# Kernel tuning notes

Hardware: AMD Instinct MI355X
Metric: run time of the kernel (lower is better)

Reference implementation:

```python
import jax, jax.numpy as jnp
import numpy as np

N = 50000      # nodes
E = 800000     # edges (before self-loops)
F_IN = 256     # num_features
H = 8          # heads (conv1)
C = 32         # hidden_size per head (conv1)
OUT = 2        # conv2 out channels (1 head)
NEG_SLOPE = 0.2


def setup_inputs() -> dict:
    key = jax.random.key(0)
    ks = jax.random.split(key, 12)
    x = jax.random.normal(ks[0], (N, F_IN), jnp.float32)
    edge_index = jax.random.randint(ks[1], (2, E), 0, N, dtype=jnp.int64)

    def glorot(k, shape):
        fan = shape[0] if len(shape) == 2 else int(np.prod(shape))
        s = float(np.sqrt(6.0 / (fan + shape[-1])))
        return jax.random.uniform(k, shape, jnp.float32, -s, s)

    W1 = glorot(ks[2], (F_IN, H * C))
    att_src1 = glorot(ks[3], (H, C))
    att_dst1 = glorot(ks[4], (H, C))
    b1 = jnp.zeros((H * C,), jnp.float32)
    W2 = glorot(ks[5], (H * C, 1 * OUT))
    att_src2 = glorot(ks[6], (1, OUT))
    att_dst2 = glorot(ks[7], (1, OUT))
    b2 = jnp.zeros((OUT,), jnp.float32)
    return {"x": x, "edge_index": edge_index, "W1": W1, "att_src1": att_src1,
            "att_dst1": att_dst1, "b1": b1, "W2": W2, "att_src2": att_src2,
            "att_dst2": att_dst2, "b2": b2}


def gat_conv(x, src, dst, W, a_src, a_dst, b, heads, ch, n):
    # x: [n, f] -> projected [n, heads, ch]
    xp = (x @ W).reshape(n, heads, ch)
    alpha_src = jnp.einsum('nhc,hc->nh', xp, a_src)   # [n, H]
    alpha_dst = jnp.einsum('nhc,hc->nh', xp, a_dst)   # [n, H]
    e = jax.nn.leaky_relu(alpha_src[src] + alpha_dst[dst], NEG_SLOPE)  # [E', H]
    # segment softmax over edges grouped by destination node
    m = jax.ops.segment_max(e, dst, num_segments=n)                    # [n, H]
    p = jnp.exp(e - m[dst])
    denom = jax.ops.segment_sum(p, dst, num_segments=n)                # [n, H]
    alpha = p / denom[dst]                                             # [E', H]
    # weighted scatter-aggregate of source messages
    out = jax.ops.segment_sum(xp[src] * alpha[:, :, None], dst, num_segments=n)
    return out.reshape(n, heads * ch) + b


def reference(x, edge_index, W1, att_src1, att_dst1, b1, W2, att_src2, att_dst2, b2):
    n = x.shape[0]
    loops = jnp.arange(n, dtype=edge_index.dtype)  # GATConv add_self_loops=True
    src = jnp.concatenate([edge_index[0], loops])
    dst = jnp.concatenate([edge_index[1], loops])
    h = jax.nn.relu(gat_conv(x, src, dst, W1, att_src1, att_dst1, b1, H, C, n))
    # eval mode: F.dropout and attention dropout are identity
    return gat_conv(h, src, dst, W2, att_src2, att_dst2, b2, 1, OUT, n)
```

## Files before the change

kernel.cpp:

```cpp
#include <hip/hip_runtime.h>
#include <math.h>

#define N_NODES 50000
#define N_EDGES 800000
#define EP (N_EDGES + N_NODES)
#define NEG 0.2f
#define SCAN_BLOCKS 49

typedef __attribute__((ext_vector_type(8))) short bf16x8;
typedef __attribute__((ext_vector_type(4))) float f32x4;

static __device__ __forceinline__ unsigned short bf16_rn(float f) {
    union { float f; unsigned int u; } v; v.f = f;
    unsigned int u = v.u;
    unsigned int r = (u + 0x7FFFu + ((u >> 16) & 1u)) >> 16;
    return (unsigned short)r;
}
static __device__ __forceinline__ float bf16_tof(unsigned short u) {
    union { unsigned int u; float f; } v; v.u = ((unsigned int)u) << 16;
    return v.f;
}


__global__ void k_hist(const int* __restrict__ ei, int* __restrict__ counts) {
    int e = blockIdx.x * 256 + threadIdx.x;
    if (e >= EP) return;
    int d = (e < N_EDGES) ? ei[N_EDGES + e] : (e - N_EDGES);
    atomicAdd(&counts[d], 1);
}

__global__ void k_scan_block(const int* __restrict__ counts, int* __restrict__ excl,
                             int* __restrict__ bsums) {
    __shared__ int wsum[4];
    int b = blockIdx.x, t = threadIdx.x;
    int lane = t & 63, w = t >> 6;
    int i0 = b * 1024 + t * 4;
    int v0 = (i0 + 0 < N_NODES) ? counts[i0 + 0] : 0;
    int v1 = (i0 + 1 < N_NODES) ? counts[i0 + 1] : 0;
    int v2 = (i0 + 2 < N_NODES) ? counts[i0 + 2] : 0;
    int v3 = (i0 + 3 < N_NODES) ? counts[i0 + 3] : 0;
    int s = v0 + v1 + v2 + v3;
    int incl = s;
    #pragma unroll
    for (int d = 1; d < 64; d <<= 1) {
        int u = __shfl_up(incl, d);
        if (lane >= d) incl += u;
    }
    if (lane == 63) wsum[w] = incl;
    __syncthreads();
    if (t == 0) {
        int run = 0;
        #pragma unroll
        for (int i = 0; i < 4; ++i) { int x = wsum[i]; wsum[i] = run; run += x; }
        bsums[b] = run;
    }
    __syncthreads();
    int base = wsum[w] + incl - s;
    if (i0 + 0 < N_NODES) excl[i0 + 0] = base;
    if (i0 + 1 < N_NODES) excl[i0 + 1] = base + v0;
    if (i0 + 2 < N_NODES) excl[i0 + 2] = base + v0 + v1;
    if (i0 + 3 < N_NODES) excl[i0 + 3] = base + v0 + v1 + v2;
}

__global__ void k_scan_mid(int* __restrict__ bsums) {
    int t = threadIdx.x;
    int v = (t < SCAN_BLOCKS) ? bsums[t] : 0;
    int incl = v;
    #pragma unroll
    for (int d = 1; d < 64; d <<= 1) {
        int u = __shfl_up(incl, d);
        if (t >= d) incl += u;
    }
    if (t < SCAN_BLOCKS) bsums[t] = incl - v;
}

__global__ void k_scan_add(int* __restrict__ row_ptr, const int* __restrict__ bsums) {
    int b = blockIdx.x, t = threadIdx.x;
    int off = bsums[b];
    int i0 = b * 1024 + t * 4;
    #pragma unroll
    for (int j = 0; j < 4; ++j)
        if (i0 + j < N_NODES) row_ptr[i0 + j] += off;
    if (b == 0 && t == 0) row_ptr[N_NODES] = EP;
}

__global__ void k_scatter(const int* __restrict__ ei, const int* __restrict__ row_ptr,
                          int* __restrict__ fill, int* __restrict__ colb) {
    int e = blockIdx.x * 256 + threadIdx.x;
    if (e >= EP) return;
    int s, d;
    if (e < N_EDGES) { s = ei[e]; d = ei[N_EDGES + e]; }
    else             { s = e - N_EDGES; d = s; }
    int pos = row_ptr[d] + atomicAdd(&fill[d], 1);
    colb[pos] = s;
}

__global__ void k_cvtW(const float* __restrict__ W1, unsigned short* __restrict__ Wt) {
    int c = blockIdx.x;
    int k = threadIdx.x;
    Wt[c * 256 + k] = bf16_rn(W1[k * 256 + c]);
}

#define GM_GRID 782
__global__ void k_gemm1m(const float* __restrict__ x, const unsigned short* __restrict__ Wt,
                         unsigned short* __restrict__ xp1b) {
    __shared__ bf16x8 lds[4 * 64 + 16 * 64];
    int t = threadIdx.x, l = t & 63, w = t >> 6;
    int rowbase = blockIdx.x * 64 + w * 16;
    int m = l & 15, kg = l >> 4;

    f32x4 acc[16];
    #pragma unroll
    for (int nt = 0; nt < 16; ++nt) acc[nt] = (f32x4){0.f, 0.f, 0.f, 0.f};

    int gra = rowbase + m;
    if (gra > N_NODES - 1) gra = N_NODES - 1;
    const float4* x4 = (const float4*)x;
    const bf16x8* WtV = (const bf16x8*)Wt;

    for (int c = 0; c < 8; ++c) {
        int k0 = c * 32;
        __syncthreads();
        {
            int fi = (gra * 256 + k0 + kg * 8) >> 2;
            float4 xa = x4[fi];
            float4 xb = x4[fi + 1];
            bf16x8 af;
            af[0] = (short)bf16_rn(xa.x); af[1] = (short)bf16_rn(xa.y);
            af[2] = (short)bf16_rn(xa.z); af[3] = (short)bf16_rn(xa.w);
            af[4] = (short)bf16_rn(xb.x); af[5] = (short)bf16_rn(xb.y);
            af[6] = (short)bf16_rn(xb.z); af[7] = (short)bf16_rn(xb.w);
            lds[w * 64 + l] = af;
        }
        #pragma unroll
        for (int q = 0; q < 4; ++q) {
            int f = t * 4 + q;
            int nt = f >> 6, fl = f & 63;
            int n = nt * 16 + (fl & 15), fkg = fl >> 4;
            lds[256 + f] = WtV[n * 32 + (k0 >> 3) + fkg];
        }
        __syncthreads();
        bf16x8 aF = lds[w * 64 + l];
        #pragma unroll
        for (int nt = 0; nt < 16; ++nt)
            acc[nt] = __builtin_amdgcn_mfma_f32_16x16x32_bf16(
                aF, lds[256 + nt * 64 + l], acc[nt], 0, 0, 0);
    }

    int cbase = l & 15, rq = l >> 4;
    #pragma unroll
    for (int reg = 0; reg < 4; ++reg) {
        int gr = rowbase + rq * 4 + reg;
        if (gr < N_NODES) {
            #pragma unroll
            for (int nt = 0; nt < 16; ++nt)
                xp1b[gr * 256 + nt * 16 + cbase] = bf16_rn(acc[nt][reg]);
        }
    }
}

__global__ void k_alphas1(const ushort4* __restrict__ xpb, const float* __restrict__ asrc,
                          const float* __restrict__ adst,
                          float* __restrict__ as1, float* __restrict__ ad1) {
    int t = threadIdx.x, l = t & 63, w = t >> 6;
    int n = blockIdx.x * 4 + w;
    ushort4 xq = xpb[n * 64 + l];
    float x0 = bf16_tof(xq.x), x1 = bf16_tof(xq.y), x2 = bf16_tof(xq.z), x3 = bf16_tof(xq.w);
    float4 a_s = ((const float4*)asrc)[l];
    float4 a_d = ((const float4*)adst)[l];
    float ds = x0 * a_s.x + x1 * a_s.y + x2 * a_s.z + x3 * a_s.w;
    float dd = x0 * a_d.x + x1 * a_d.y + x2 * a_d.z + x3 * a_d.w;
    #pragma unroll
    for (int m = 1; m < 8; m <<= 1) {
        ds += __shfl_xor(ds, m);
        dd += __shfl_xor(dd, m);
    }
    if ((l & 7) == 0) {
        int h = l >> 3;
        as1[n * 8 + h] = ds;
        ad1[n * 8 + h] = dd;
    }
}

__global__ void k_agg1(const ushort4* __restrict__ xpb, const float* __restrict__ as1,
                       const float* __restrict__ ad1, const int* __restrict__ row_ptr,
                       const int* __restrict__ colb, const float* __restrict__ b1,
                       float* __restrict__ hout) {
    int t = threadIdx.x, l = t & 63, w = t >> 6;
    int n = blockIdx.x * 4 + w;
    int hidx = l >> 3;
    float adn = ad1[n * 8 + hidx];
    int start = row_ptr[n], end = row_ptr[n + 1];
    float4 acc = {0.f, 0.f, 0.f, 0.f};
    float den = 0.f;
    int j = start;
    for (; j + 4 <= end; j += 4) {
        int s0 = colb[j], s1 = colb[j + 1], s2 = colb[j + 2], s3 = colb[j + 3];
        ushort4 x0 = xpb[s0 * 64 + l];
        ushort4 x1 = xpb[s1 * 64 + l];
        ushort4 x2 = xpb[s2 * 64 + l];
        ushort4 x3 = xpb[s3 * 64 + l];
        float e0 = as1[s0 * 8 + hidx] + adn;
        float e1 = as1[s1 * 8 + hidx] + adn;
        float e2 = as1[s2 * 8 + hidx] + adn;
        float e3 = as1[s3 * 8 + hidx] + adn;
        e0 = (e0 > 0.f) ? e0 : NEG * e0;
        e1 = (e1 > 0.f) ? e1 : NEG * e1;
        e2 = (e2 > 0.f) ? e2 : NEG * e2;
        e3 = (e3 > 0.f) ? e3 : NEG * e3;
        float p0 = __expf(e0), p1 = __expf(e1), p2 = __expf(e2), p3 = __expf(e3);
        den += (p0 + p1) + (p2 + p3);
        acc.x = fmaf(p0, bf16_tof(x0.x), acc.x);
        acc.y = fmaf(p0, bf16_tof(x0.y), acc.y);
        acc.z = fmaf(p0, bf16_tof(x0.z), acc.z);
        acc.w = fmaf(p0, bf16_tof(x0.w), acc.w);
        acc.x = fmaf(p1, bf16_tof(x1.x), acc.x);
        acc.y = fmaf(p1, bf16_tof(x1.y), acc.y);
        acc.z = fmaf(p1, bf16_tof(x1.z), acc.z);
        acc.w = fmaf(p1, bf16_tof(x1.w), acc.w);
        acc.x = fmaf(p2, bf16_tof(x2.x), acc.x);
        acc.y = fmaf(p2, bf16_tof(x2.y), acc.y);
        acc.z = fmaf(p2, bf16_tof(x2.z), acc.z);
        acc.w = fmaf(p2, bf16_tof(x2.w), acc.w);
        acc.x = fmaf(p3, bf16_tof(x3.x), acc.x);
        acc.y = fmaf(p3, bf16_tof(x3.y), acc.y);
        acc.z = fmaf(p3, bf16_tof(x3.z), acc.z);
        acc.w = fmaf(p3, bf16_tof(x3.w), acc.w);
    }
    for (; j < end; ++j) {
        int s = colb[j];
        ushort4 xv = xpb[s * 64 + l];
        float e = as1[s * 8 + hidx] + adn;
        e = (e > 0.f) ? e : NEG * e;
        float p = __expf(e);
        den += p;
        acc.x = fmaf(p, bf16_tof(xv.x), acc.x);
        acc.y = fmaf(p, bf16_tof(xv.y), acc.y);
        acc.z = fmaf(p, bf16_tof(xv.z), acc.z);
        acc.w = fmaf(p, bf16_tof(xv.w), acc.w);
    }
    float4 bv = ((const float4*)b1)[l];
    float inv = 1.f / den;
    float4 o;
    o.x = fmaxf(acc.x * inv + bv.x, 0.f);
    o.y = fmaxf(acc.y * inv + bv.y, 0.f);
    o.z = fmaxf(acc.z * inv + bv.z, 0.f);
    o.w = fmaxf(acc.w * inv + bv.w, 0.f);
    ((float4*)hout)[n * 64 + l] = o;
}

__global__ void k_proj2(const float* __restrict__ h, const float* __restrict__ W2,
                        const float* __restrict__ as2w, const float* __restrict__ ad2w,
                        float* __restrict__ xp2, float* __restrict__ as2,
                        float* __restrict__ ad2) {
    int t = threadIdx.x, l = t & 63, w = t >> 6;
    int n = blockIdx.x * 4 + w;
    float4 hv = ((const float4*)h)[n * 64 + l];
    float4 wa = ((const float4*)W2)[2 * l];
    float4 wb = ((const float4*)W2)[2 * l + 1];
    float d0 = hv.x * wa.x + hv.y * wa.z + hv.z * wb.x + hv.w * wb.z;
    float d1 = hv.x * wa.y + hv.y * wa.w + hv.z * wb.y + hv.w * wb.w;
    #pragma unroll
    for (int m = 1; m < 64; m <<= 1) {
        d0 += __shfl_xor(d0, m);
        d1 += __shfl_xor(d1, m);
    }
    if (l == 0) {
        xp2[2 * n] = d0;
        xp2[2 * n + 1] = d1;
        as2[n] = d0 * as2w[0] + d1 * as2w[1];
        ad2[n] = d0 * ad2w[0] + d1 * ad2w[1];
    }
}

__global__ void k_agg2(const float* __restrict__ xp2, const float* __restrict__ as2,
                       const float* __restrict__ ad2, const int* __restrict__ row_ptr,
                       const int* __restrict__ colb, const float* __restrict__ b2,
                       float* __restrict__ out) {
    int t = threadIdx.x, l = t & 63, w = t >> 6;
    int n = blockIdx.x * 4 + w;
    int start = row_ptr[n], end = row_ptr[n + 1];
    float adn = ad2[n];
    float a0 = 0.f, a1 = 0.f, den = 0.f;
    for (int j = start + l; j < end; j += 64) {
        int s = colb[j];
        float e = as2[s] + adn;
        e = (e > 0.f) ? e : NEG * e;
        float p = __expf(e);
        den += p;
        a0 = fmaf(p, xp2[2 * s], a0);
        a1 = fmaf(p, xp2[2 * s + 1], a1);
    }
    #pragma unroll
    for (int m = 1; m < 64; m <<= 1) {
        a0 += __shfl_xor(a0, m);
        a1 += __shfl_xor(a1, m);
        den += __shfl_xor(den, m);
    }
    if (l == 0) {
        out[2 * n] = a0 / den + b2[0];
        out[2 * n + 1] = a1 / den + b2[1];
    }
}

extern "C" void kernel_launch(void* const* d_in, const int* in_sizes, int n_in,
                              void* d_out, int out_size, void* d_ws, size_t ws_size,
                              hipStream_t stream) {
    const float* x     = (const float*)d_in[0];
    const int*   ei    = (const int*)d_in[1];
    const float* W1    = (const float*)d_in[2];
    const float* asrc1 = (const float*)d_in[3];
    const float* adst1 = (const float*)d_in[4];
    const float* b1    = (const float*)d_in[5];
    const float* W2    = (const float*)d_in[6];
    const float* asrc2 = (const float*)d_in[7];
    const float* adst2 = (const float*)d_in[8];
    const float* b2    = (const float*)d_in[9];
    float* out = (float*)d_out;

    char* ws = (char*)d_ws;
    unsigned short* xp1b = (unsigned short*)(ws + 0);
    unsigned short* Wt   = (unsigned short*)(ws + 25600000);
    float* hbuf    = (float*)(ws + 51200000);
    float* as1     = (float*)(ws + 102400000);
    float* ad1     = (float*)(ws + 104000000);
    float* xp2     = (float*)(ws + 105600000);
    float* as2     = (float*)(ws + 106000000);
    float* ad2     = (float*)(ws + 106200000);
    int*   counts  = (int*)  (ws + 106400000);
    int*   fill    = (int*)  (ws + 106600000);
    int*   row_ptr = (int*)  (ws + 106800000);
    int*   colb    = (int*)  (ws + 107000064);
    int*   bsums   = (int*)  (ws + 110400064);

    hipMemsetAsync(counts, 0, 400000, stream);

    int egrid = (EP + 255) / 256;
    k_hist      <<<egrid,       256, 0, stream>>>(ei, counts);
    k_scan_block<<<SCAN_BLOCKS, 256, 0, stream>>>(counts, row_ptr, bsums);
    k_scan_mid  <<<1,            64, 0, stream>>>(bsums);
    k_scan_add  <<<SCAN_BLOCKS, 256, 0, stream>>>(row_ptr, bsums);
    k_scatter   <<<egrid,       256, 0, stream>>>(ei, row_ptr, fill, colb);

    k_cvtW      <<<256,    256, 0, stream>>>(W1, Wt);
    k_gemm1m    <<<GM_GRID, 256, 0, stream>>>(x, Wt, xp1b);
    k_alphas1   <<<12500,  256, 0, stream>>>((const ushort4*)xp1b, asrc1, adst1, as1, ad1);
    k_agg1      <<<12500,  256, 0, stream>>>((const ushort4*)xp1b, as1, ad1, row_ptr, colb, b1, hbuf);
    k_proj2     <<<12500,  256, 0, stream>>>(hbuf, W2, asrc2, adst2, xp2, as2, ad2);
    k_agg2      <<<12500,  256, 0, stream>>>(xp2, as2, ad2, row_ptr, colb, b2, out);
}
```

Baseline: 322.6 us.

## Fuse layer-2 projection into agg1 and drop LDS staging in GEMM

The layer-2 projection and attention-logit computation now run at the end of the layer-1 aggregation kernel. This removes the 51 MB fp32 hidden buffer write and read-back and one kernel launch. The layer-1 GEMM also stops staging x and W tiles through LDS with block barriers: each wave now loads its A fragment directly and reads B fragments from global memory, which should be cache-resident. In exchange, B traffic from global/L2 is redundant across waves, while the barrier stalls go away.

```diff
diff --git a/kernel.cpp b/kernel.cpp
--- a/kernel.cpp
+++ b/kernel.cpp
@@ -102,9 +102,9 @@
 }
 
 #define GM_GRID 782
-__global__ void k_gemm1m(const float* __restrict__ x, const unsigned short* __restrict__ Wt,
-                         unsigned short* __restrict__ xp1b) {
-    __shared__ bf16x8 lds[4 * 64 + 16 * 64];
+__global__ __launch_bounds__(256) void
+k_gemm1m(const float* __restrict__ x, const unsigned short* __restrict__ Wt,
+         unsigned short* __restrict__ xp1b) {
     int t = threadIdx.x, l = t & 63, w = t >> 6;
     int rowbase = blockIdx.x * 64 + w * 16;
     int m = l & 15, kg = l >> 4;
@@ -118,33 +118,22 @@
     const float4* x4 = (const float4*)x;
     const bf16x8* WtV = (const bf16x8*)Wt;
 
+    #pragma unroll 2
     for (int c = 0; c < 8; ++c) {
         int k0 = c * 32;
-        __syncthreads();
-        {
-            int fi = (gra * 256 + k0 + kg * 8) >> 2;
-            float4 xa = x4[fi];
-            float4 xb = x4[fi + 1];
-            bf16x8 af;
-            af[0] = (short)bf16_rn(xa.x); af[1] = (short)bf16_rn(xa.y);
-            af[2] = (short)bf16_rn(xa.z); af[3] = (short)bf16_rn(xa.w);
-            af[4] = (short)bf16_rn(xb.x); af[5] = (short)bf16_rn(xb.y);
-            af[6] = (short)bf16_rn(xb.z); af[7] = (short)bf16_rn(xb.w);
-            lds[w * 64 + l] = af;
+        int fi = (gra * 256 + k0 + kg * 8) >> 2;
+        float4 xa = x4[fi];
+        float4 xb = x4[fi + 1];
+        bf16x8 aF;
+        aF[0] = (short)bf16_rn(xa.x); aF[1] = (short)bf16_rn(xa.y);
+        aF[2] = (short)bf16_rn(xa.z); aF[3] = (short)bf16_rn(xa.w);
+        aF[4] = (short)bf16_rn(xb.x); aF[5] = (short)bf16_rn(xb.y);
+        aF[6] = (short)bf16_rn(xb.z); aF[7] = (short)bf16_rn(xb.w);
+        #pragma unroll
+        for (int nt = 0; nt < 16; ++nt) {
+            bf16x8 bF = WtV[(nt * 16 + m) * 32 + c * 4 + kg];
+            acc[nt] = __builtin_amdgcn_mfma_f32_16x16x32_bf16(aF, bF, acc[nt], 0, 0, 0);
         }
-        #pragma unroll
-        for (int q = 0; q < 4; ++q) {
-            int f = t * 4 + q;
-            int nt = f >> 6, fl = f & 63;
-            int n = nt * 16 + (fl & 15), fkg = fl >> 4;
-            lds[256 + f] = WtV[n * 32 + (k0 >> 3) + fkg];
-        }
-        __syncthreads();
-        bf16x8 aF = lds[w * 64 + l];
-        #pragma unroll
-        for (int nt = 0; nt < 16; ++nt)
-            acc[nt] = __builtin_amdgcn_mfma_f32_16x16x32_bf16(
-                aF, lds[256 + nt * 64 + l], acc[nt], 0, 0, 0);
     }
 
     int cbase = l & 15, rq = l >> 4;
@@ -185,7 +174,10 @@
 __global__ void k_agg1(const ushort4* __restrict__ xpb, const float* __restrict__ as1,
                        const float* __restrict__ ad1, const int* __restrict__ row_ptr,
                        const int* __restrict__ colb, const float* __restrict__ b1,
-                       float* __restrict__ hout) {
+                       const float* __restrict__ W2, const float* __restrict__ as2w,
+                       const float* __restrict__ ad2w,
+                       float* __restrict__ xp2, float* __restrict__ as2,
+                       float* __restrict__ ad2) {
     int t = threadIdx.x, l = t & 63, w = t >> 6;
     int n = blockIdx.x * 4 + w;
     int hidx = l >> 3;
@@ -246,20 +238,10 @@
     o.y = fmaxf(acc.y * inv + bv.y, 0.f);
     o.z = fmaxf(acc.z * inv + bv.z, 0.f);
     o.w = fmaxf(acc.w * inv + bv.w, 0.f);
-    ((float4*)hout)[n * 64 + l] = o;
-}
-
-__global__ void k_proj2(const float* __restrict__ h, const float* __restrict__ W2,
-                        const float* __restrict__ as2w, const float* __restrict__ ad2w,
-                        float* __restrict__ xp2, float* __restrict__ as2,
-                        float* __restrict__ ad2) {
-    int t = threadIdx.x, l = t & 63, w = t >> 6;
-    int n = blockIdx.x * 4 + w;
-    float4 hv = ((const float4*)h)[n * 64 + l];
     float4 wa = ((const float4*)W2)[2 * l];
     float4 wb = ((const float4*)W2)[2 * l + 1];
-    float d0 = hv.x * wa.x + hv.y * wa.z + hv.z * wb.x + hv.w * wb.z;
-    float d1 = hv.x * wa.y + hv.y * wa.w + hv.z * wb.y + hv.w * wb.w;
+    float d0 = o.x * wa.x + o.y * wa.z + o.z * wb.x + o.w * wb.z;
+    float d1 = o.x * wa.y + o.y * wa.w + o.z * wb.y + o.w * wb.w;
     #pragma unroll
     for (int m = 1; m < 64; m <<= 1) {
         d0 += __shfl_xor(d0, m);
@@ -321,7 +303,6 @@
     char* ws = (char*)d_ws;
     unsigned short* xp1b = (unsigned short*)(ws + 0);
     unsigned short* Wt   = (unsigned short*)(ws + 25600000);
-    float* hbuf    = (float*)(ws + 51200000);
     float* as1     = (float*)(ws + 102400000);
     float* ad1     = (float*)(ws + 104000000);
     float* xp2     = (float*)(ws + 105600000);
@@ -345,7 +326,7 @@
     k_cvtW      <<<256,    256, 0, stream>>>(W1, Wt);
     k_gemm1m    <<<GM_GRID, 256, 0, stream>>>(x, Wt, xp1b);
     k_alphas1   <<<12500,  256, 0, stream>>>((const ushort4*)xp1b, asrc1, adst1, as1, ad1);
-    k_agg1      <<<12500,  256, 0, stream>>>((const ushort4*)xp1b, as1, ad1, row_ptr, colb, b1, hbuf);
-    k_proj2     <<<12500,  256, 0, stream>>>(hbuf, W2, asrc2, adst2, xp2, as2, ad2);
+    k_agg1      <<<12500,  256, 0, stream>>>((const ushort4*)xp1b, as1, ad1, row_ptr, colb,
+                                             b1, W2, asrc2, adst2, xp2, as2, ad2);
     k_agg2      <<<12500,  256, 0, stream>>>(xp2, as2, ad2, row_ptr, colb, b2, out);
 }
```

Measured after the change: 347.6 us. +7.7%, slower.
